# Optimization experiments

Measured on AMD Instinct MI355X. Metric: run time of the kernel, lower is better.

Reference implementation:

```python
import jax, jax.numpy as jnp
from jax import lax
import numpy as np

B, F, T, D, H = 16, 20, 128, 300, 256

def _lstm_scan(x, mask, W, U, b):
    # x: [N, T, D], mask: [N, T] bool. Keras gate order: i, f, g(c), o.
    N = x.shape[0]
    xz = jnp.einsum('ntd,dh->nth', x, W) + b  # [N, T, 4H] input projection, hoisted out of scan
    def step(carry, inp):
        h, c = carry
        z_x, m = inp
        z = z_x + h @ U
        i, f, g, o = jnp.split(z, 4, axis=-1)
        c_new = jax.nn.sigmoid(f) * c + jax.nn.sigmoid(i) * jnp.tanh(g)
        h_new = jax.nn.sigmoid(o) * jnp.tanh(c_new)
        m = m[:, None]
        # Keras masking: masked steps copy previous state/output through
        h = jnp.where(m, h_new, h)
        c = jnp.where(m, c_new, c)
        return (h, c), h
    init = (jnp.zeros((N, H), x.dtype), jnp.zeros((N, H), x.dtype))
    _, hs = lax.scan(step, init, (jnp.swapaxes(xz, 0, 1), jnp.swapaxes(mask, 0, 1)))
    return jnp.swapaxes(hs, 0, 1)  # [N, T, H]

def setup_inputs() -> dict:
    key = jax.random.key(0)
    ks = jax.random.split(key, 8)
    facts = jax.random.normal(ks[0], (B, F, T, D), dtype=jnp.float32)
    lengths = jax.random.randint(ks[1], (B, F), T // 2, T + 1)
    mask = jnp.arange(T)[None, None, :] < lengths[..., None]  # valid-prefix padding mask [B,F,T]
    s_in = 1.0 / np.sqrt(D)
    s_h = 1.0 / np.sqrt(H)
    W_fwd = jax.random.normal(ks[2], (D, 4 * H), dtype=jnp.float32) * s_in
    U_fwd = jax.random.normal(ks[3], (H, 4 * H), dtype=jnp.float32) * s_h
    b_fwd = jnp.zeros((4 * H,), dtype=jnp.float32).at[H:2 * H].set(1.0)  # unit forget bias
    W_bwd = jax.random.normal(ks[4], (D, 4 * H), dtype=jnp.float32) * s_in
    U_bwd = jax.random.normal(ks[5], (H, 4 * H), dtype=jnp.float32) * s_h
    b_bwd = jnp.zeros((4 * H,), dtype=jnp.float32).at[H:2 * H].set(1.0)
    return {"facts": facts, "mask": mask, "W_fwd": W_fwd, "U_fwd": U_fwd, "b_fwd": b_fwd,
            "W_bwd": W_bwd, "U_bwd": U_bwd, "b_bwd": b_bwd}

def reference(facts, mask, W_fwd, U_fwd, b_fwd, W_bwd, U_bwd, b_bwd):
    # Flatten (B, F) -> N sequences, as in FactEncoder.call
    x = facts.reshape(B * F, T, D)
    m = mask.reshape(B * F, T)
    h_f = _lstm_scan(x, m, W_fwd, U_fwd, b_fwd)
    # Bidirectional backward branch: reverse time, run, reverse output back
    h_b = _lstm_scan(x[:, ::-1], m[:, ::-1], W_bwd, U_bwd, b_bwd)[:, ::-1]
    out = jnp.concatenate([h_f, h_b], axis=-1)  # merge_mode='concat'
    return out.reshape(B, F, T, 2 * H)
```

## Files before the change

kernel.cpp:

```cpp
#include <hip/hip_runtime.h>
#include <hip/hip_bf16.h>

constexpr int Bc   = 16;
constexpr int Fc   = 20;
constexpr int T    = 128;
constexpr int D    = 300;
constexpr int H    = 256;
constexpr int NSEQ = Bc * Fc;
constexpr int G4   = 4 * H;
constexpr int DP   = 320;

constexpr int WTN = 2 * G4 * DP;
constexpr int UTN = 2 * G4 * H;

typedef __attribute__((ext_vector_type(8))) short  short8_t;
typedef __attribute__((ext_vector_type(4))) float  f32x4;

__device__ __forceinline__ short8_t ld8(const short* p) { return *(const short8_t*)p; }
__device__ __forceinline__ f32x4 mf(short8_t a, short8_t b, f32x4 c) {
    return __builtin_amdgcn_mfma_f32_16x16x32_bf16(a, b, c, 0, 0, 0);
}
__device__ __forceinline__ float b2f(short s) {
    unsigned u = ((unsigned)(unsigned short)s) << 16;
    return __builtin_bit_cast(float, u);
}
__device__ __forceinline__ short f2b(float f) {
    unsigned u = __builtin_bit_cast(unsigned, f);
    u += 0x7fffu + ((u >> 16) & 1u);
    return (short)(u >> 16);
}
__device__ __forceinline__ float blo(unsigned w) { return __builtin_bit_cast(float, w << 16); }
__device__ __forceinline__ float bhi(unsigned w) { return __builtin_bit_cast(float, w & 0xffff0000u); }
__device__ __forceinline__ float sigf(float x) {
    float e = __builtin_amdgcn_exp2f(x * -1.44269504f);
    return __builtin_amdgcn_rcpf(1.0f + e);
}
__device__ __forceinline__ float tanhf_(float x) {
    float e = __builtin_amdgcn_exp2f(x * -2.88539008f);
    return __builtin_amdgcn_rcpf(1.0f + e) * 2.0f - 1.0f;
}
__device__ __forceinline__ bool in_is_fp32(const unsigned* bfw) {
    return bfw[256] == 0x3F800000u;
}
__device__ __forceinline__ float in_val(const void* p, long long i, bool is32) {
    return is32 ? ((const float*)p)[i] : b2f(((const short*)p)[i]);
}

__global__ void prep_wu(const void* __restrict__ Wf, const void* __restrict__ Uf,
                        const void* __restrict__ Wb, const void* __restrict__ Ub,
                        const unsigned* __restrict__ bfw,
                        short* __restrict__ wt, short* __restrict__ ut)
{
    const bool is32 = in_is_fp32(bfw);
    int idx = blockIdx.x * 256 + threadIdx.x;
    if (idx < WTN) {
        int d_ = idx / (G4 * DP), j = idx - d_ * (G4 * DP);
        int n  = j / DP, k = j - n * DP;
        const void* W = d_ ? Wb : Wf;
        wt[idx] = (k < D) ? f2b(in_val(W, (long long)k * G4 + n, is32)) : (short)0;
    } else if (idx < WTN + UTN) {
        int i  = idx - WTN;
        int d_ = i / (G4 * H), j = i - d_ * (G4 * H);
        int n  = j / H, k = j - n * H;
        const void* U = d_ ? Ub : Uf;
        int kp = (k & ~31) | ((k & 15) << 1) | ((k >> 4) & 1);
        ut[i - k + kp] = f2b(in_val(U, (long long)k * G4 + n, is32));
    }
}

__global__ void prep_xp(const void* __restrict__ facts, const unsigned* __restrict__ bfw,
                        short* __restrict__ xpc, int Tc, int t00, int t01)
{
    const bool is32 = in_is_fp32(bfw);
    long long total = 2LL * NSEQ * Tc * DP;
    long long idx = (long long)blockIdx.x * 256 + threadIdx.x;
    if (idx >= total) return;
    int perdir = NSEQ * Tc * DP;
    int d_  = (int)(idx / perdir);
    int rem = (int)(idx - (long long)d_ * perdir);
    int seq = rem / (Tc * DP);
    int r2  = rem - seq * (Tc * DP);
    int tl  = r2 / DP;
    int k   = r2 - tl * DP;
    int t0  = d_ ? t01 : t00;
    long long frow = (long long)(seq * T + t0 + tl) * D;
    xpc[idx] = (k < D) ? f2b(in_val(facts, frow + k, is32)) : (short)0;
}

__global__ void gemm_xz(const short* __restrict__ xpc, const short* __restrict__ wt,
                        const void* __restrict__ bfv, const void* __restrict__ bbv,
                        const unsigned* __restrict__ bfw,
                        short* __restrict__ xzc, int Tc)
{
    const bool is32 = in_is_fp32(bfw);
    const int dir = blockIdx.z;
    const short* wtd  = wt + (size_t)dir * G4 * DP;
    const void*  bias = dir ? bbv : bfv;
    const short* xpA = xpc + (size_t)dir * NSEQ * Tc * DP + (size_t)blockIdx.y * 128 * DP;
    short* xzd = xzc + (size_t)dir * NSEQ * Tc * G4;

    const int m0 = blockIdx.y * 128;
    const int n0 = blockIdx.x * 128;
    const int tid = threadIdx.x;
    const int wid = tid >> 6, lane = tid & 63, quad = lane >> 4, l15 = lane & 15;
    const int wm = wid >> 1, wn = wid & 1;

    __shared__ __align__(16) short Al[128 * 40];
    __shared__ __align__(16) short Bl[128 * 40];

    const short* wtB = wtd + (size_t)n0 * DP;

    f32x4 acc[4][4];
#pragma unroll
    for (int mi = 0; mi < 4; ++mi)
#pragma unroll
        for (int ni = 0; ni < 4; ++ni) acc[mi][ni] = (f32x4){0.f, 0.f, 0.f, 0.f};

    for (int kk = 0; kk < 10; ++kk) {
#pragma unroll
        for (int i = 0; i < 2; ++i) {
            int cid = tid + i * 256;
            int row = cid >> 2, cc = cid & 3;
            *(short8_t*)&Al[row * 40 + cc * 8] = ld8(xpA + (size_t)row * DP + kk * 32 + cc * 8);
            *(short8_t*)&Bl[row * 40 + cc * 8] = ld8(wtB + (size_t)row * DP + kk * 32 + cc * 8);
        }
        __syncthreads();
        short8_t a[4], b[4];
#pragma unroll
        for (int mi = 0; mi < 4; ++mi)
            a[mi] = ld8(&Al[(wm * 64 + mi * 16 + l15) * 40 + quad * 8]);
#pragma unroll
        for (int ni = 0; ni < 4; ++ni)
            b[ni] = ld8(&Bl[(wn * 64 + ni * 16 + l15) * 40 + quad * 8]);
#pragma unroll
        for (int mi = 0; mi < 4; ++mi)
#pragma unroll
            for (int ni = 0; ni < 4; ++ni)
                acc[mi][ni] = mf(a[mi], b[ni], acc[mi][ni]);
        __syncthreads();
    }

#pragma unroll
    for (int ni = 0; ni < 4; ++ni) {
        int col = n0 + wn * 64 + ni * 16 + l15;
        float bv = is32 ? ((const float*)bias)[col] : b2f(((const short*)bias)[col]);
        int pos = (col & ~31) | ((col & 15) << 1) | ((col >> 4) & 1);
#pragma unroll
        for (int mi = 0; mi < 4; ++mi) {
            int row = m0 + wm * 64 + mi * 16 + quad * 4;
#pragma unroll
            for (int r = 0; r < 4; ++r)
                xzd[(size_t)(row + r) * G4 + pos] = f2b(acc[mi][ni][r] + bv);
        }
    }
}

__global__ __launch_bounds__(512, 2)
void lstm_chunk(const short* __restrict__ xzc, const short* __restrict__ utp,
                const void* __restrict__ maskp, void* __restrict__ out,
                const unsigned* __restrict__ bfw,
                short* __restrict__ h_ws, float* __restrict__ c_ws,
                int Tc, int cbase, int first)
{
    const bool is32 = in_is_fp32(bfw);
    const int tid = threadIdx.x;
    const int wv = tid >> 6, lane = tid & 63, quad = lane >> 4, l15 = lane & 15;
    const int g = blockIdx.x;
    const int dir = g / 20, s0 = (g % 20) * 16;

    const short* ut  = utp + (size_t)dir * G4 * H;
    const short* xzd = xzc + (size_t)dir * NSEQ * Tc * G4;

    constexpr int HR = 296;
    __shared__ __align__(16) short hbuf[2][16 * HR];
    __shared__ __align__(16) short ulds[8 * 2 * 8 * 64 * 8];
    __shared__ __align__(4) unsigned char mbuf[T * 16];

    {
        const unsigned* mw = (const unsigned*)maskp;
        unsigned w0 = mw[0];
        int mode = (w0 == 1u || w0 == 0x3F800000u) ? 0 : (w0 == 0x3F803F80u ? 1 : 2);
        for (int i = tid; i < T * 16; i += 512) {
            int t = i >> 4, sq = i & 15;
            int gi = (s0 + sq) * T + t;
            unsigned char mv;
            if (mode == 0)      mv = (mw[gi] != 0) ? 1 : 0;
            else if (mode == 1) mv = (((const unsigned short*)maskp)[gi] != 0) ? 1 : 0;
            else                mv = ((const unsigned char*)maskp)[gi];
            mbuf[i] = mv;
        }
    }

    const int fb = l15 * H + quad * 8;
    const int c4 = (2 * 256 + 32 * wv +  0) * H + fb;
    const int c7 = (3 * 256 + 32 * wv + 16) * H + fb;

    short8_t ureg[4][8];
    {
        const int cr[4] = { (0*256 + 32*wv +  0) * H + fb,
                            (0*256 + 32*wv + 16) * H + fb,
                            (1*256 + 32*wv +  0) * H + fb,
                            (1*256 + 32*wv + 16) * H + fb };
#pragma unroll
        for (int a = 0; a < 4; ++a)
#pragma unroll
            for (int kk = 0; kk < 8; ++kk)
                ureg[a][kk] = ld8(ut + cr[a] + kk * 32);
    }
#pragma unroll
    for (int a = 0; a < 4; ++a)
#pragma unroll
        for (int kk = 0; kk < 8; ++kk)
            asm volatile("" : "+v"(ureg[a][kk]));

    {
        const int c5 = (2 * 256 + 32 * wv + 16) * H + fb;
        const int c6 = (3 * 256 + 32 * wv +  0) * H + fb;
#pragma unroll
        for (int kk = 0; kk < 8; ++kk) {
            *(short8_t*)&ulds[(((wv * 2 + 0) * 8 + kk) * 64 + lane) * 8] = ld8(ut + c5 + kk * 32);
            *(short8_t*)&ulds[(((wv * 2 + 1) * 8 + kk) * 64 + lane) * 8] = ld8(ut + c6 + kk * 32);
        }
    }

    for (int i = tid; i < 16 * 256; i += 512) {
        int sq = i >> 8, d = i & 255;
        int pos = (d & ~31) | ((d & 15) << 1) | ((d >> 4) & 1);
        hbuf[0][sq * HR + pos] = first ? (short)0
            : h_ws[(size_t)(dir * NSEQ + s0 + sq) * H + d];
    }
    float cst[2][4], hst[2][4];
#pragma unroll
    for (int jj = 0; jj < 2; ++jj)
#pragma unroll
        for (int r = 0; r < 4; ++r) {
            size_t sidx = (size_t)(dir * NSEQ + s0 + quad * 4 + r) * H + 32 * wv + 16 * jj + l15;
            hst[jj][r] = first ? 0.f : b2f(h_ws[sidx]);
            cst[jj][r] = first ? 0.f : c_ws[sidx];
        }

    const int dstep = dir ? -1 : 1;
    const int tl0 = dir ? (Tc - 1) : 0;
    const int tg0 = dir ? (T - 1 - cbase) : cbase;

    const unsigned* xzu = (const unsigned*)xzd;
    const int seqb = s0 + quad * 4;
    int xzo0 = (seqb * Tc + tl0) * 512 + 16 * wv + l15;
    int ob0  = (seqb * T + tg0) * (2 * H) + dir * H + 32 * wv + l15;

    short8_t u4[4], u7[4];
#pragma unroll
    for (int i = 0; i < 4; ++i) {
        u4[i] = ld8(ut + c4 + i * 32);
        u7[i] = ld8(ut + c7 + i * 32);
    }

    __syncthreads();

    int p = 0;
    for (int s = 0; s < Tc; ++s) {
        const int t = dir ? (T - 1 - cbase - s) : (cbase + s);

        f32x4 acc[8];
#pragma unroll
        for (int a = 0; a < 8; ++a) acc[a] = (f32x4){0.f, 0.f, 0.f, 0.f};

        unsigned xzv[4][4];
#pragma unroll
        for (int gi = 0; gi < 4; ++gi)
#pragma unroll
            for (int r = 0; r < 4; ++r)
                xzv[gi][r] = xzu[xzo0 + r * (Tc * 512) + gi * 128];

        const short* hb = &hbuf[p][0];
        __builtin_amdgcn_s_setprio(1);
#pragma unroll
        for (int kk = 0; kk < 8; ++kk) {
            short8_t af = ld8(&hb[l15 * HR + kk * 32 + quad * 8]);
#pragma unroll
            for (int a = 0; a < 4; ++a) acc[a] = mf(af, ureg[a][kk], acc[a]);
            short8_t u5 = ld8(&ulds[(((wv * 2 + 0) * 8 + kk) * 64 + lane) * 8]);
            acc[5] = mf(af, u5, acc[5]);
            short8_t u6 = ld8(&ulds[(((wv * 2 + 1) * 8 + kk) * 64 + lane) * 8]);
            acc[6] = mf(af, u6, acc[6]);
            acc[4] = mf(af, u4[kk & 3], acc[4]);
            acc[7] = mf(af, u7[kk & 3], acc[7]);
            u4[kk & 3] = ld8(ut + c4 + (((kk + 4) & 7) * 32));
            u7[kk & 3] = ld8(ut + c7 + (((kk + 4) & 7) * 32));
        }
        __builtin_amdgcn_s_setprio(0);

        const unsigned mw4 = *(const unsigned*)&mbuf[t * 16 + quad * 4];

#pragma unroll
        for (int r = 0; r < 4; ++r) {
            bool m = ((mw4 >> (8 * r)) & 0xffu) != 0;
#pragma unroll
            for (int jj = 0; jj < 2; ++jj) {
                float xi = jj ? bhi(xzv[0][r]) : blo(xzv[0][r]);
                float xf = jj ? bhi(xzv[1][r]) : blo(xzv[1][r]);
                float xg = jj ? bhi(xzv[2][r]) : blo(xzv[2][r]);
                float xo = jj ? bhi(xzv[3][r]) : blo(xzv[3][r]);
                float zi = acc[0 + jj][r] + xi;
                float zf = acc[2 + jj][r] + xf;
                float zg = acc[4 + jj][r] + xg;
                float zo = acc[6 + jj][r] + xo;
                float iv = sigf(zi), fv = sigf(zf), gv = tanhf_(zg), ov = sigf(zo);
                float cn = fv * cst[jj][r] + iv * gv;
                float hn = ov * tanhf_(cn);
                cst[jj][r] = m ? cn : cst[jj][r];
                hst[jj][r] = m ? hn : hst[jj][r];
            }
            unsigned hw = (unsigned)(unsigned short)f2b(hst[0][r])
                        | ((unsigned)(unsigned short)f2b(hst[1][r]) << 16);
            *(unsigned*)&hbuf[p ^ 1][(quad * 4 + r) * HR + 32 * wv + 2 * l15] = hw;
            int ob = ob0 + r * (T * 2 * H);
            if (is32) {
                ((float*)out)[ob]      = hst[0][r];
                ((float*)out)[ob + 16] = hst[1][r];
            } else {
                ((short*)out)[ob]      = (short)(hw & 0xffffu);
                ((short*)out)[ob + 16] = (short)(hw >> 16);
            }
        }
        xzo0 += dstep * 512;
        ob0  += dstep * 512;
        p ^= 1;
        asm volatile("s_waitcnt lgkmcnt(0)" ::: "memory");
        __builtin_amdgcn_s_barrier();
        __builtin_amdgcn_sched_barrier(0);
    }

#pragma unroll
    for (int jj = 0; jj < 2; ++jj)
#pragma unroll
        for (int r = 0; r < 4; ++r) {
            size_t sidx = (size_t)(dir * NSEQ + s0 + quad * 4 + r) * H + 32 * wv + 16 * jj + l15;
            h_ws[sidx] = f2b(hst[jj][r]);
            c_ws[sidx] = cst[jj][r];
        }
}

extern "C" void kernel_launch(void* const* d_in, const int* in_sizes, int n_in,
                              void* d_out, int out_size, void* d_ws, size_t ws_size,
                              hipStream_t stream)
{
    const void* facts = d_in[0];
    const void* maskp = d_in[1];
    const void* Wf = d_in[2];
    const void* Uf = d_in[3];
    const void* bf = d_in[4];
    const void* Wb = d_in[5];
    const void* Ub = d_in[6];
    const void* bb = d_in[7];
    const unsigned* bfw = (const unsigned*)bf;

    const unsigned long long fixedB =
        (unsigned long long)(WTN + UTN) * 2 + (2ull * NSEQ * H) * 2 + (2ull * NSEQ * H) * 4 + 1024;
    int Tc = 128;
    while (Tc > 4 && (1720320ull * Tc + fixedB) > ws_size) Tc >>= 1;
    const int nC = T / Tc;

    short* ws   = (short*)d_ws;
    short* xzc  = ws;
    short* xpc  = xzc + (size_t)2 * NSEQ * Tc * G4;
    short* wt   = xpc + (size_t)2 * NSEQ * Tc * DP;
    short* ut   = wt + WTN;
    short* h_ws = ut + UTN;
    float* c_ws = (float*)(h_ws + (size_t)2 * NSEQ * H);

    prep_wu<<<(WTN + UTN + 255) / 256, 256, 0, stream>>>(Wf, Uf, Wb, Ub, bfw, wt, ut);

    const long long xpTotal = 2LL * NSEQ * Tc * DP;
    for (int c = 0; c < nC; ++c) {
        int t00 = c * Tc;
        int t01 = T - (c + 1) * Tc;
        prep_xp<<<(int)((xpTotal + 255) / 256), 256, 0, stream>>>(facts, bfw, xpc, Tc, t00, t01);
        gemm_xz<<<dim3(8, NSEQ * Tc / 128, 2), 256, 0, stream>>>(xpc, wt, bf, bb, bfw, xzc, Tc);
        lstm_chunk<<<40, 512, 0, stream>>>(xzc, ut, maskp, d_out, bfw, h_ws, c_ws,
                                           Tc, c * Tc, c == 0 ? 1 : 0);
    }
}
```

Measured before the change: 871.5 us.

## Split LSTM recurrence across 16 waves per block with interleaved gate layout

The recurrent kernel now runs 1024 threads (16 waves) per block instead of 512. Each wave owns 16 hidden units and computes all four gates for them, so per-wave MFMA work and register-held U fragments are halved. The xz projection output is re-laid out so the four gates of a hidden unit sit contiguously and load as one 8-byte read, and that load is moved inside the MFMA loop to hide latency. The h buffer drops its permuted layout. Costs are more waves contending at the per-step barrier and narrower scalar output stores.

```diff
diff --git a/kernel.cpp b/kernel.cpp
--- a/kernel.cpp
+++ b/kernel.cpp
@@ -15,6 +15,7 @@
 
 typedef __attribute__((ext_vector_type(8))) short  short8_t;
 typedef __attribute__((ext_vector_type(4))) float  f32x4;
+typedef __attribute__((ext_vector_type(2))) unsigned uint2_t;
 
 __device__ __forceinline__ short8_t ld8(const short* p) { return *(const short8_t*)p; }
 __device__ __forceinline__ f32x4 mf(short8_t a, short8_t b, f32x4 c) {
@@ -63,8 +64,7 @@
         int d_ = i / (G4 * H), j = i - d_ * (G4 * H);
         int n  = j / H, k = j - n * H;
         const void* U = d_ ? Ub : Uf;
-        int kp = (k & ~31) | ((k & 15) << 1) | ((k >> 4) & 1);
-        ut[i - k + kp] = f2b(in_val(U, (long long)k * G4 + n, is32));
+        ut[i] = f2b(in_val(U, (long long)k * G4 + n, is32));
     }
 }
 
@@ -144,7 +144,7 @@
     for (int ni = 0; ni < 4; ++ni) {
         int col = n0 + wn * 64 + ni * 16 + l15;
         float bv = is32 ? ((const float*)bias)[col] : b2f(((const short*)bias)[col]);
-        int pos = (col & ~31) | ((col & 15) << 1) | ((col >> 4) & 1);
+        int pos = ((col & 255) << 2) | (col >> 8);
 #pragma unroll
         for (int mi = 0; mi < 4; ++mi) {
             int row = m0 + wm * 64 + mi * 16 + quad * 4;
@@ -155,7 +155,7 @@
     }
 }
 
-__global__ __launch_bounds__(512, 2)
+__global__ __launch_bounds__(1024, 4)
 void lstm_chunk(const short* __restrict__ xzc, const short* __restrict__ utp,
                 const void* __restrict__ maskp, void* __restrict__ out,
                 const unsigned* __restrict__ bfw,
@@ -165,6 +165,8 @@
     const bool is32 = in_is_fp32(bfw);
     const int tid = threadIdx.x;
     const int wv = tid >> 6, lane = tid & 63, quad = lane >> 4, l15 = lane & 15;
+    const int WV = wv >> 1, half = wv & 1;
+    const int cb = 32 * WV + 16 * half;
     const int g = blockIdx.x;
     const int dir = g / 20, s0 = (g % 20) * 16;
 
@@ -173,14 +175,14 @@
 
     constexpr int HR = 296;
     __shared__ __align__(16) short hbuf[2][16 * HR];
-    __shared__ __align__(16) short ulds[8 * 2 * 8 * 64 * 8];
+    __shared__ __align__(16) short ulds[16 * 8 * 64 * 8];
     __shared__ __align__(4) unsigned char mbuf[T * 16];
 
     {
         const unsigned* mw = (const unsigned*)maskp;
         unsigned w0 = mw[0];
         int mode = (w0 == 1u || w0 == 0x3F800000u) ? 0 : (w0 == 0x3F803F80u ? 1 : 2);
-        for (int i = tid; i < T * 16; i += 512) {
+        for (int i = tid; i < T * 16; i += 1024) {
             int t = i >> 4, sq = i & 15;
             int gi = (s0 + sq) * T + t;
             unsigned char mv;
@@ -192,68 +194,57 @@
     }
 
     const int fb = l15 * H + quad * 8;
-    const int c4 = (2 * 256 + 32 * wv +  0) * H + fb;
-    const int c7 = (3 * 256 + 32 * wv + 16) * H + fb;
-
-    short8_t ureg[4][8];
+    const int c3 = (3 * 256 + cb) * H + fb;
+
+    short8_t ureg[2][8];
     {
-        const int cr[4] = { (0*256 + 32*wv +  0) * H + fb,
-                            (0*256 + 32*wv + 16) * H + fb,
-                            (1*256 + 32*wv +  0) * H + fb,
-                            (1*256 + 32*wv + 16) * H + fb };
-#pragma unroll
-        for (int a = 0; a < 4; ++a)
+        const int cr[2] = { (0 * 256 + cb) * H + fb,
+                            (1 * 256 + cb) * H + fb };
+#pragma unroll
+        for (int a = 0; a < 2; ++a)
 #pragma unroll
             for (int kk = 0; kk < 8; ++kk)
                 ureg[a][kk] = ld8(ut + cr[a] + kk * 32);
     }
 #pragma unroll
-    for (int a = 0; a < 4; ++a)
+    for (int a = 0; a < 2; ++a)
 #pragma unroll
         for (int kk = 0; kk < 8; ++kk)
             asm volatile("" : "+v"(ureg[a][kk]));
 
     {
-        const int c5 = (2 * 256 + 32 * wv + 16) * H + fb;
-        const int c6 = (3 * 256 + 32 * wv +  0) * H + fb;
-#pragma unroll
-        for (int kk = 0; kk < 8; ++kk) {
-            *(short8_t*)&ulds[(((wv * 2 + 0) * 8 + kk) * 64 + lane) * 8] = ld8(ut + c5 + kk * 32);
-            *(short8_t*)&ulds[(((wv * 2 + 1) * 8 + kk) * 64 + lane) * 8] = ld8(ut + c6 + kk * 32);
-        }
-    }
-
-    for (int i = tid; i < 16 * 256; i += 512) {
+        const int c2 = (2 * 256 + cb) * H + fb;
+#pragma unroll
+        for (int kk = 0; kk < 8; ++kk)
+            *(short8_t*)&ulds[((wv * 8 + kk) * 64 + lane) * 8] = ld8(ut + c2 + kk * 32);
+    }
+
+    for (int i = tid; i < 16 * 256; i += 1024) {
         int sq = i >> 8, d = i & 255;
-        int pos = (d & ~31) | ((d & 15) << 1) | ((d >> 4) & 1);
-        hbuf[0][sq * HR + pos] = first ? (short)0
+        hbuf[0][sq * HR + d] = first ? (short)0
             : h_ws[(size_t)(dir * NSEQ + s0 + sq) * H + d];
     }
-    float cst[2][4], hst[2][4];
-#pragma unroll
-    for (int jj = 0; jj < 2; ++jj)
-#pragma unroll
-        for (int r = 0; r < 4; ++r) {
-            size_t sidx = (size_t)(dir * NSEQ + s0 + quad * 4 + r) * H + 32 * wv + 16 * jj + l15;
-            hst[jj][r] = first ? 0.f : b2f(h_ws[sidx]);
-            cst[jj][r] = first ? 0.f : c_ws[sidx];
-        }
+    float cst[4], hst[4];
+#pragma unroll
+    for (int r = 0; r < 4; ++r) {
+        size_t sidx = (size_t)(dir * NSEQ + s0 + quad * 4 + r) * H + cb + l15;
+        hst[r] = first ? 0.f : b2f(h_ws[sidx]);
+        cst[r] = first ? 0.f : c_ws[sidx];
+    }
 
     const int dstep = dir ? -1 : 1;
     const int tl0 = dir ? (Tc - 1) : 0;
     const int tg0 = dir ? (T - 1 - cbase) : cbase;
 
-    const unsigned* xzu = (const unsigned*)xzd;
+    const uint2_t* xzu = (const uint2_t*)xzd;
     const int seqb = s0 + quad * 4;
-    int xzo0 = (seqb * Tc + tl0) * 512 + 16 * wv + l15;
-    int ob0  = (seqb * T + tg0) * (2 * H) + dir * H + 32 * wv + l15;
-
-    short8_t u4[4], u7[4];
-#pragma unroll
-    for (int i = 0; i < 4; ++i) {
-        u4[i] = ld8(ut + c4 + i * 32);
-        u7[i] = ld8(ut + c7 + i * 32);
-    }
+    const int dim = cb + l15;
+    int xzo0 = (seqb * Tc + tl0) * 256 + dim;
+    int ob0  = (seqb * T + tg0) * (2 * H) + dir * H + dim;
+
+    short8_t u3r[4];
+#pragma unroll
+    for (int i = 0; i < 4; ++i) u3r[i] = ld8(ut + c3 + i * 32);
 
     __syncthreads();
 
@@ -261,32 +252,27 @@
     for (int s = 0; s < Tc; ++s) {
         const int t = dir ? (T - 1 - cbase - s) : (cbase + s);
 
-        f32x4 acc[8];
-#pragma unroll
-        for (int a = 0; a < 8; ++a) acc[a] = (f32x4){0.f, 0.f, 0.f, 0.f};
-
-        unsigned xzv[4][4];
-#pragma unroll
-        for (int gi = 0; gi < 4; ++gi)
-#pragma unroll
-            for (int r = 0; r < 4; ++r)
-                xzv[gi][r] = xzu[xzo0 + r * (Tc * 512) + gi * 128];
+        f32x4 acc[4];
+#pragma unroll
+        for (int a = 0; a < 4; ++a) acc[a] = (f32x4){0.f, 0.f, 0.f, 0.f};
+        uint2_t xzv[4];
 
         const short* hb = &hbuf[p][0];
         __builtin_amdgcn_s_setprio(1);
 #pragma unroll
         for (int kk = 0; kk < 8; ++kk) {
             short8_t af = ld8(&hb[l15 * HR + kk * 32 + quad * 8]);
-#pragma unroll
-            for (int a = 0; a < 4; ++a) acc[a] = mf(af, ureg[a][kk], acc[a]);
-            short8_t u5 = ld8(&ulds[(((wv * 2 + 0) * 8 + kk) * 64 + lane) * 8]);
-            acc[5] = mf(af, u5, acc[5]);
-            short8_t u6 = ld8(&ulds[(((wv * 2 + 1) * 8 + kk) * 64 + lane) * 8]);
-            acc[6] = mf(af, u6, acc[6]);
-            acc[4] = mf(af, u4[kk & 3], acc[4]);
-            acc[7] = mf(af, u7[kk & 3], acc[7]);
-            u4[kk & 3] = ld8(ut + c4 + (((kk + 4) & 7) * 32));
-            u7[kk & 3] = ld8(ut + c7 + (((kk + 4) & 7) * 32));
+            acc[0] = mf(af, ureg[0][kk], acc[0]);
+            acc[1] = mf(af, ureg[1][kk], acc[1]);
+            short8_t u2 = ld8(&ulds[((wv * 8 + kk) * 64 + lane) * 8]);
+            acc[2] = mf(af, u2, acc[2]);
+            acc[3] = mf(af, u3r[kk & 3], acc[3]);
+            u3r[kk & 3] = ld8(ut + c3 + (((kk + 4) & 7) * 32));
+            if (kk == 2) {
+#pragma unroll
+                for (int r = 0; r < 4; ++r)
+                    xzv[r] = xzu[xzo0 + r * (Tc * 256)];
+            }
         }
         __builtin_amdgcn_s_setprio(0);
 
@@ -295,35 +281,22 @@
 #pragma unroll
         for (int r = 0; r < 4; ++r) {
             bool m = ((mw4 >> (8 * r)) & 0xffu) != 0;
-#pragma unroll
-            for (int jj = 0; jj < 2; ++jj) {
-                float xi = jj ? bhi(xzv[0][r]) : blo(xzv[0][r]);
-                float xf = jj ? bhi(xzv[1][r]) : blo(xzv[1][r]);
-                float xg = jj ? bhi(xzv[2][r]) : blo(xzv[2][r]);
-                float xo = jj ? bhi(xzv[3][r]) : blo(xzv[3][r]);
-                float zi = acc[0 + jj][r] + xi;
-                float zf = acc[2 + jj][r] + xf;
-                float zg = acc[4 + jj][r] + xg;
-                float zo = acc[6 + jj][r] + xo;
-                float iv = sigf(zi), fv = sigf(zf), gv = tanhf_(zg), ov = sigf(zo);
-                float cn = fv * cst[jj][r] + iv * gv;
-                float hn = ov * tanhf_(cn);
-                cst[jj][r] = m ? cn : cst[jj][r];
-                hst[jj][r] = m ? hn : hst[jj][r];
-            }
-            unsigned hw = (unsigned)(unsigned short)f2b(hst[0][r])
-                        | ((unsigned)(unsigned short)f2b(hst[1][r]) << 16);
-            *(unsigned*)&hbuf[p ^ 1][(quad * 4 + r) * HR + 32 * wv + 2 * l15] = hw;
+            float zi = acc[0][r] + blo(xzv[r].x);
+            float zf = acc[1][r] + bhi(xzv[r].x);
+            float zg = acc[2][r] + blo(xzv[r].y);
+            float zo = acc[3][r] + bhi(xzv[r].y);
+            float iv = sigf(zi), fv = sigf(zf), gv = tanhf_(zg), ov = sigf(zo);
+            float cn = fv * cst[r] + iv * gv;
+            float hn = ov * tanhf_(cn);
+            cst[r] = m ? cn : cst[r];
+            hst[r] = m ? hn : hst[r];
+            short h16 = f2b(hst[r]);
+            hbuf[p ^ 1][(quad * 4 + r) * HR + dim] = h16;
             int ob = ob0 + r * (T * 2 * H);
-            if (is32) {
-                ((float*)out)[ob]      = hst[0][r];
-                ((float*)out)[ob + 16] = hst[1][r];
-            } else {
-                ((short*)out)[ob]      = (short)(hw & 0xffffu);
-                ((short*)out)[ob + 16] = (short)(hw >> 16);
-            }
-        }
-        xzo0 += dstep * 512;
+            if (is32) ((float*)out)[ob] = hst[r];
+            else      ((short*)out)[ob] = h16;
+        }
+        xzo0 += dstep * 256;
         ob0  += dstep * 512;
         p ^= 1;
         asm volatile("s_waitcnt lgkmcnt(0)" ::: "memory");
@@ -332,13 +305,11 @@
     }
 
 #pragma unroll
-    for (int jj = 0; jj < 2; ++jj)
-#pragma unroll
-        for (int r = 0; r < 4; ++r) {
-            size_t sidx = (size_t)(dir * NSEQ + s0 + quad * 4 + r) * H + 32 * wv + 16 * jj + l15;
-            h_ws[sidx] = f2b(hst[jj][r]);
-            c_ws[sidx] = cst[jj][r];
-        }
+    for (int r = 0; r < 4; ++r) {
+        size_t sidx = (size_t)(dir * NSEQ + s0 + quad * 4 + r) * H + cb + l15;
+        h_ws[sidx] = f2b(hst[r]);
+        c_ws[sidx] = cst[r];
+    }
 }
 
 extern "C" void kernel_launch(void* const* d_in, const int* in_sizes, int n_in,
@@ -377,7 +348,7 @@
         int t01 = T - (c + 1) * Tc;
         prep_xp<<<(int)((xpTotal + 255) / 256), 256, 0, stream>>>(facts, bfw, xpc, Tc, t00, t01);
         gemm_xz<<<dim3(8, NSEQ * Tc / 128, 2), 256, 0, stream>>>(xpc, wt, bf, bb, bfw, xzc, Tc);
-        lstm_chunk<<<40, 512, 0, stream>>>(xzc, ut, maskp, d_out, bfw, h_ws, c_ws,
-                                           Tc, c * Tc, c == 0 ? 1 : 0);
-    }
-}
+        lstm_chunk<<<40, 1024, 0, stream>>>(xzc, ut, maskp, d_out, bfw, h_ws, c_ws,
+                                            Tc, c * Tc, c == 0 ? 1 : 0);
+    }
+}
```

Result: slower. 1.030 ms (+18.2%).

## Skew recurrent step into two half-ticks overlapping matmul with gate math

Applied to the files above, without the earlier changes.

Splits each recurrent time step into two half-ticks, one for even rows and one for odd rows. Each half-tick runs the full h·U MFMA loop, then applies the gate nonlinearities to one half of the rows using accumulators saved from the previous tick. It also prefetches the input-projection values one tick ahead and moves a different gate slice of U into LDS, streaming the rest from global with a shorter prefetch ring. The aim is to hide the dependency between the matmul and the elementwise update, at the cost of issuing roughly twice as many MFMA passes per time step.

```diff
diff --git a/kernel.cpp b/kernel.cpp
--- a/kernel.cpp
+++ b/kernel.cpp
@@ -1,5 +1,6 @@
 #include <hip/hip_runtime.h>
 #include <hip/hip_bf16.h>
+#include <type_traits>
 
 constexpr int Bc   = 16;
 constexpr int Fc   = 20;
@@ -192,7 +193,7 @@
     }
 
     const int fb = l15 * H + quad * 8;
-    const int c4 = (2 * 256 + 32 * wv +  0) * H + fb;
+    const int c6 = (3 * 256 + 32 * wv +  0) * H + fb;
     const int c7 = (3 * 256 + 32 * wv + 16) * H + fb;
 
     short8_t ureg[4][8];
@@ -214,12 +215,12 @@
             asm volatile("" : "+v"(ureg[a][kk]));
 
     {
+        const int c4 = (2 * 256 + 32 * wv +  0) * H + fb;
         const int c5 = (2 * 256 + 32 * wv + 16) * H + fb;
-        const int c6 = (3 * 256 + 32 * wv +  0) * H + fb;
 #pragma unroll
         for (int kk = 0; kk < 8; ++kk) {
-            *(short8_t*)&ulds[(((wv * 2 + 0) * 8 + kk) * 64 + lane) * 8] = ld8(ut + c5 + kk * 32);
-            *(short8_t*)&ulds[(((wv * 2 + 1) * 8 + kk) * 64 + lane) * 8] = ld8(ut + c6 + kk * 32);
+            *(short8_t*)&ulds[(((wv * 2 + 0) * 8 + kk) * 64 + lane) * 8] = ld8(ut + c4 + kk * 32);
+            *(short8_t*)&ulds[(((wv * 2 + 1) * 8 + kk) * 64 + lane) * 8] = ld8(ut + c5 + kk * 32);
         }
     }
 
@@ -245,33 +246,30 @@
 
     const unsigned* xzu = (const unsigned*)xzd;
     const int seqb = s0 + quad * 4;
-    int xzo0 = (seqb * Tc + tl0) * 512 + 16 * wv + l15;
-    int ob0  = (seqb * T + tg0) * (2 * H) + dir * H + 32 * wv + l15;
-
-    short8_t u4[4], u7[4];
-#pragma unroll
-    for (int i = 0; i < 4; ++i) {
-        u4[i] = ld8(ut + c4 + i * 32);
-        u7[i] = ld8(ut + c7 + i * 32);
-    }
+    const int xzbase = (seqb * Tc + tl0) * 512 + 16 * wv + l15;
+    int xzoA = xzbase, xzoB = xzbase;
+    int obA = (seqb * T + tg0) * (2 * H) + dir * H + 32 * wv + l15;
+    int obB = obA;
+
+    short8_t u6r[2], u7r[2];
+    u6r[0] = ld8(ut + c6);      u6r[1] = ld8(ut + c6 + 32);
+    u7r[0] = ld8(ut + c7);      u7r[1] = ld8(ut + c7 + 32);
+
+    unsigned xzn[4][2];
+#pragma unroll
+    for (int gi = 0; gi < 4; ++gi)
+#pragma unroll
+        for (int ri = 0; ri < 2; ++ri)
+            xzn[gi][ri] = xzu[xzoA + (0 + 2 * ri) * (Tc * 512) + gi * 128];
+    xzoA += dstep * 512;
 
     __syncthreads();
 
     int p = 0;
-    for (int s = 0; s < Tc; ++s) {
-        const int t = dir ? (T - 1 - cbase - s) : (cbase + s);
-
-        f32x4 acc[8];
-#pragma unroll
-        for (int a = 0; a < 8; ++a) acc[a] = (f32x4){0.f, 0.f, 0.f, 0.f};
-
-        unsigned xzv[4][4];
-#pragma unroll
-        for (int gi = 0; gi < 4; ++gi)
-#pragma unroll
-            for (int r = 0; r < 4; ++r)
-                xzv[gi][r] = xzu[xzo0 + r * (Tc * 512) + gi * 128];
-
+    int tcur = 0;
+    float accP[8][2];
+
+    auto kloop = [&](f32x4 (&acc)[8]) {
         const short* hb = &hbuf[p][0];
         __builtin_amdgcn_s_setprio(1);
 #pragma unroll
@@ -279,32 +277,50 @@
             short8_t af = ld8(&hb[l15 * HR + kk * 32 + quad * 8]);
 #pragma unroll
             for (int a = 0; a < 4; ++a) acc[a] = mf(af, ureg[a][kk], acc[a]);
-            short8_t u5 = ld8(&ulds[(((wv * 2 + 0) * 8 + kk) * 64 + lane) * 8]);
-            acc[5] = mf(af, u5, acc[5]);
-            short8_t u6 = ld8(&ulds[(((wv * 2 + 1) * 8 + kk) * 64 + lane) * 8]);
-            acc[6] = mf(af, u6, acc[6]);
-            acc[4] = mf(af, u4[kk & 3], acc[4]);
-            acc[7] = mf(af, u7[kk & 3], acc[7]);
-            u4[kk & 3] = ld8(ut + c4 + (((kk + 4) & 7) * 32));
-            u7[kk & 3] = ld8(ut + c7 + (((kk + 4) & 7) * 32));
+            short8_t g0 = ld8(&ulds[(((wv * 2 + 0) * 8 + kk) * 64 + lane) * 8]);
+            acc[4] = mf(af, g0, acc[4]);
+            short8_t g1 = ld8(&ulds[(((wv * 2 + 1) * 8 + kk) * 64 + lane) * 8]);
+            acc[5] = mf(af, g1, acc[5]);
+            acc[6] = mf(af, u6r[kk & 1], acc[6]);
+            acc[7] = mf(af, u7r[kk & 1], acc[7]);
+            u6r[kk & 1] = ld8(ut + c6 + (((kk + 2) & 7) * 32));
+            u7r[kk & 1] = ld8(ut + c7 + (((kk + 2) & 7) * 32));
         }
         __builtin_amdgcn_s_setprio(0);
-
-        const unsigned mw4 = *(const unsigned*)&mbuf[t * 16 + quad * 4];
-
-#pragma unroll
-        for (int r = 0; r < 4; ++r) {
+    };
+
+    {
+        f32x4 acc[8];
+#pragma unroll
+        for (int a = 0; a < 8; ++a) acc[a] = (f32x4){0.f, 0.f, 0.f, 0.f};
+        kloop(acc);
+#pragma unroll
+        for (int a = 0; a < 8; ++a) { accP[a][0] = acc[a][0]; accP[a][1] = acc[a][2]; }
+    }
+
+    auto tick = [&](auto PIc) {
+        constexpr int PI = decltype(PIc)::value;
+        f32x4 acc[8];
+#pragma unroll
+        for (int a = 0; a < 8; ++a) acc[a] = (f32x4){0.f, 0.f, 0.f, 0.f};
+        kloop(acc);
+
+        const unsigned mw4 = *(const unsigned*)&mbuf[tcur * 16 + quad * 4];
+        int& obP = PI ? obB : obA;
+#pragma unroll
+        for (int ri = 0; ri < 2; ++ri) {
+            const int r = PI + 2 * ri;
             bool m = ((mw4 >> (8 * r)) & 0xffu) != 0;
 #pragma unroll
             for (int jj = 0; jj < 2; ++jj) {
-                float xi = jj ? bhi(xzv[0][r]) : blo(xzv[0][r]);
-                float xf = jj ? bhi(xzv[1][r]) : blo(xzv[1][r]);
-                float xg = jj ? bhi(xzv[2][r]) : blo(xzv[2][r]);
-                float xo = jj ? bhi(xzv[3][r]) : blo(xzv[3][r]);
-                float zi = acc[0 + jj][r] + xi;
-                float zf = acc[2 + jj][r] + xf;
-                float zg = acc[4 + jj][r] + xg;
-                float zo = acc[6 + jj][r] + xo;
+                float xi = jj ? bhi(xzn[0][ri]) : blo(xzn[0][ri]);
+                float xf = jj ? bhi(xzn[1][ri]) : blo(xzn[1][ri]);
+                float xg = jj ? bhi(xzn[2][ri]) : blo(xzn[2][ri]);
+                float xo = jj ? bhi(xzn[3][ri]) : blo(xzn[3][ri]);
+                float zi = accP[0 + jj][ri] + xi;
+                float zf = accP[2 + jj][ri] + xf;
+                float zg = accP[4 + jj][ri] + xg;
+                float zo = accP[6 + jj][ri] + xo;
                 float iv = sigf(zi), fv = sigf(zf), gv = tanhf_(zg), ov = sigf(zo);
                 float cn = fv * cst[jj][r] + iv * gv;
                 float hn = ov * tanhf_(cn);
@@ -314,7 +330,7 @@
             unsigned hw = (unsigned)(unsigned short)f2b(hst[0][r])
                         | ((unsigned)(unsigned short)f2b(hst[1][r]) << 16);
             *(unsigned*)&hbuf[p ^ 1][(quad * 4 + r) * HR + 32 * wv + 2 * l15] = hw;
-            int ob = ob0 + r * (T * 2 * H);
+            int ob = obP + r * (T * 2 * H);
             if (is32) {
                 ((float*)out)[ob]      = hst[0][r];
                 ((float*)out)[ob + 16] = hst[1][r];
@@ -323,12 +339,40 @@
                 ((short*)out)[ob + 16] = (short)(hw >> 16);
             }
         }
-        xzo0 += dstep * 512;
-        ob0  += dstep * 512;
+        obP += dstep * 512;
+
+#pragma unroll
+        for (int ri = 0; ri < 2; ++ri) {
+            const int rC = (PI ^ 1) + 2 * ri;
+            unsigned hw = (unsigned)(unsigned short)f2b(hst[0][rC])
+                        | ((unsigned)(unsigned short)f2b(hst[1][rC]) << 16);
+            *(unsigned*)&hbuf[p ^ 1][(quad * 4 + rC) * HR + 32 * wv + 2 * l15] = hw;
+        }
+
+#pragma unroll
+        for (int a = 0; a < 8; ++a) {
+            accP[a][0] = acc[a][(PI ^ 1)];
+            accP[a][1] = acc[a][(PI ^ 1) + 2];
+        }
+
+        int& xzoQ = PI ? xzoA : xzoB;
+#pragma unroll
+        for (int gi = 0; gi < 4; ++gi)
+#pragma unroll
+            for (int ri = 0; ri < 2; ++ri)
+                xzn[gi][ri] = xzu[xzoQ + ((PI ^ 1) + 2 * ri) * (Tc * 512) + gi * 128];
+        xzoQ += dstep * 512;
+
         p ^= 1;
         asm volatile("s_waitcnt lgkmcnt(0)" ::: "memory");
         __builtin_amdgcn_s_barrier();
         __builtin_amdgcn_sched_barrier(0);
+    };
+
+    for (int n = 0; n < Tc; ++n) {
+        tcur = dir ? (T - 1 - cbase - n) : (cbase + n);
+        tick(std::integral_constant<int, 0>{});
+        tick(std::integral_constant<int, 1>{});
     }
 
 #pragma unroll
```

After: 1.655 ms. 1.9x slower.
